# Optimization experiments

Measured on AMD Instinct MI355X. Metric: run time of the kernel, lower is better.

The kernel has to match this reference:

```python
import jax, jax.numpy as jnp
import numpy as np

N_NODES = 100000
N_EDGES = 1600000
F_IN = 128
HID = 128
N_CLASSES = 32
N_GRAPHS = 512


def _seg_mean(vals, idx, num_segments):
    s = jax.ops.segment_sum(vals, idx, num_segments=num_segments)
    cnt = jax.ops.segment_sum(jnp.ones((vals.shape[0],), vals.dtype), idx, num_segments=num_segments)
    return s / jnp.maximum(cnt, 1.0)[:, None]


def _sage_conv(x, src, dst, Wl, bl, Wr):
    # PyG SAGEConv(mean): out = lin_l(mean_{j in N(i)} x_j) + lin_r(x_i); lin_l has bias, lin_r does not.
    agg = _seg_mean(x[src], dst, N_NODES)          # gather + scatter-mean  [N, d]
    return agg @ Wl.T + bl + x @ Wr.T              # [N, H]


def setup_inputs() -> dict:
    key = jax.random.key(0)
    ks = jax.random.split(key, 16)
    x = jax.random.normal(ks[0], (N_NODES, F_IN), dtype=jnp.float32)
    edge_index = jax.random.randint(ks[1], (2, N_EDGES), 0, N_NODES, dtype=jnp.int64)
    batch = jnp.sort(jax.random.randint(ks[2], (N_NODES,), 0, N_GRAPHS, dtype=jnp.int64))
    sc = 0.05
    params = {
        'Wl0': jax.random.normal(ks[3], (HID, F_IN), jnp.float32) * sc,
        'bl0': jnp.zeros((HID,), jnp.float32),
        'Wr0': jax.random.normal(ks[4], (HID, F_IN), jnp.float32) * sc,
        'Wl1': jax.random.normal(ks[5], (HID, HID), jnp.float32) * sc,
        'bl1': jnp.zeros((HID,), jnp.float32),
        'Wr1': jax.random.normal(ks[6], (HID, HID), jnp.float32) * sc,
        'Wl2': jax.random.normal(ks[7], (HID, HID), jnp.float32) * sc,
        'bl2': jnp.zeros((HID,), jnp.float32),
        'Wr2': jax.random.normal(ks[8], (HID, HID), jnp.float32) * sc,
        'Wlin': jax.random.normal(ks[9], (N_CLASSES, HID), jnp.float32) * sc,
        'blin': jnp.zeros((N_CLASSES,), jnp.float32),
    }
    return {'x': x, 'edge_index': edge_index, 'batch': batch, **params}


def reference(x, edge_index, batch, Wl0, bl0, Wr0, Wl1, bl1, Wr1, Wl2, bl2, Wr2, Wlin, blin):
    src, dst = edge_index[0], edge_index[1]
    # GraphSAGE backbone: relu between layers, no act after last (out_channels set); dropout=identity in eval.
    h = jax.nn.relu(_sage_conv(x, src, dst, Wl0, bl0, Wr0))
    h = jax.nn.relu(_sage_conv(h, src, dst, Wl1, bl1, Wr1))
    h = _sage_conv(h, src, dst, Wl2, bl2, Wr2)
    # global_mean_pool over batch index -> [n_graphs, HID]
    g = _seg_mean(h, batch, N_GRAPHS)
    return g @ Wlin.T + blin  # [n_graphs, n_classes]
```

## Files before the change

kernel.cpp:

```cpp
#include <hip/hip_runtime.h>
#include <hip/hip_bf16.h>


typedef __attribute__((ext_vector_type(8))) short short8v;
typedef __attribute__((ext_vector_type(4))) float f32x4;

#define RK_CH 12544
#define RK_NS 64

__device__ __forceinline__ unsigned short f2bf(float f) {
    __hip_bfloat16 h = __float2bfloat16(f);
    return *reinterpret_cast<unsigned short*>(&h);
}
__device__ __forceinline__ float bf_lo(unsigned u) { return __uint_as_float(u << 16); }
__device__ __forceinline__ float bf_hi(unsigned u) { return __uint_as_float(u & 0xffff0000u); }
__device__ __forceinline__ unsigned packbf(float lo, float hi) {
    return ((unsigned)f2bf(hi) << 16) | f2bf(lo);
}


__launch_bounds__(256)
__global__ void pre_kernel(const int* __restrict__ dst,
                           unsigned short* __restrict__ rank16,
                           unsigned short* __restrict__ counts16,
                           int nE, int nChunk, int es,
                           const float* __restrict__ x, unsigned short* __restrict__ xbf, int x4,
                           const float* __restrict__ w0, const float* __restrict__ w1,
                           const float* __restrict__ w2, const float* __restrict__ w3,
                           const float* __restrict__ w4, const float* __restrict__ w5,
                           unsigned short* __restrict__ o0, unsigned short* __restrict__ o1,
                           unsigned short* __restrict__ o2, unsigned short* __restrict__ o3,
                           unsigned short* __restrict__ o4, unsigned short* __restrict__ o5,
                           int w4n, int w4b) {
    __shared__ unsigned cnt[RK_CH];
    int rhB  = nChunk * RK_NS;
    int cvtB = (x4 + 255) / 256;
    int bid  = blockIdx.x;

    if (bid < rhB) {
        int s = bid / nChunk;
        int c = bid % nChunk;
        int lo = c * RK_CH;
        for (int i = threadIdx.x; i < RK_CH; i += 256) cnt[i] = 0u;
        __syncthreads();

        int ebeg = s * es;
        int eend = ebeg + es; if (eend > nE) eend = nE;
        if (ebeg < eend) {
            int nvec = (eend - ebeg) >> 2;
            for (int g = threadIdx.x; g < nvec; g += 256) {
                int e = ebeg + g * 4;
                int4 d4 = *(const int4*)&dst[e];
                unsigned dc;
                dc = (unsigned)(d4.x - lo);
                if (dc < RK_CH) rank16[e]     = (unsigned short)atomicAdd(&cnt[dc], 1u);
                dc = (unsigned)(d4.y - lo);
                if (dc < RK_CH) rank16[e + 1] = (unsigned short)atomicAdd(&cnt[dc], 1u);
                dc = (unsigned)(d4.z - lo);
                if (dc < RK_CH) rank16[e + 2] = (unsigned short)atomicAdd(&cnt[dc], 1u);
                dc = (unsigned)(d4.w - lo);
                if (dc < RK_CH) rank16[e + 3] = (unsigned short)atomicAdd(&cnt[dc], 1u);
            }
            for (int e = ebeg + (nvec << 2) + threadIdx.x; e < eend; e += 256) {
                unsigned dc = (unsigned)(dst[e] - lo);
                if (dc < RK_CH) rank16[e] = (unsigned short)atomicAdd(&cnt[dc], 1u);
            }
        }
        __syncthreads();
        size_t base = ((size_t)(c * RK_NS + s)) * RK_CH;
        for (int i = threadIdx.x; i < RK_CH; i += 256)
            counts16[base + i] = (unsigned short)cnt[i];
    } else if (bid < rhB + cvtB) {
        int i = (bid - rhB) * 256 + threadIdx.x;
        if (i < x4) {
            float4 v = ((const float4*)x)[i];
            ushort4 o;
            o.x = f2bf(v.x); o.y = f2bf(v.y); o.z = f2bf(v.z); o.w = f2bf(v.w);
            ((ushort4*)xbf)[i] = o;
        }
    } else {
        int idx  = bid - rhB - cvtB;
        int wsel = idx / w4b;
        int wb   = idx % w4b;
        const float* in; unsigned short* out;
        switch (wsel) {
            case 0: in = w0; out = o0; break;
            case 1: in = w1; out = o1; break;
            case 2: in = w2; out = o2; break;
            case 3: in = w3; out = o3; break;
            case 4: in = w4; out = o4; break;
            default: in = w5; out = o5; break;
        }
        int i = wb * 256 + threadIdx.x;
        if (i < w4n) {
            float4 v = ((const float4*)in)[i];
            ushort4 o;
            o.x = f2bf(v.x); o.y = f2bf(v.y); o.z = f2bf(v.z); o.w = f2bf(v.w);
            ((ushort4*)out)[i] = o;
        }
    }
}


__launch_bounds__(1024)
__global__ void seg_scan1_kernel(unsigned short* __restrict__ counts16,
                                 int* __restrict__ rowptr, int* __restrict__ bsum, int n) {
    __shared__ int s[1024];
    int lid = threadIdx.x;
    int d = blockIdx.x * 1024 + lid;
    int v = 0;
    if (d < n) {
        int c = d / RK_CH;
        int i = d - c * RK_CH;
        size_t base = ((size_t)c * RK_NS) * RK_CH + i;
        unsigned run = 0;
        for (int sl = 0; sl < RK_NS; ++sl) {
            size_t idx = base + (size_t)sl * RK_CH;
            unsigned t = counts16[idx];
            counts16[idx] = (unsigned short)run;
            run += t;
        }
        v = (int)run;
    }
    s[lid] = v;
    __syncthreads();
    #pragma unroll
    for (int off = 1; off < 1024; off <<= 1) {
        int t = (lid >= off) ? s[lid - off] : 0;
        __syncthreads();
        s[lid] += t;
        __syncthreads();
    }
    if (d < n) rowptr[d] = s[lid] - v;
    if (lid == 0) bsum[blockIdx.x] = s[1023];
}

__global__ void scan2_kernel(int* __restrict__ bsum, int nb) {
    __shared__ int s[1024];
    int lid = threadIdx.x;
    int v = (lid < nb) ? bsum[lid] : 0;
    s[lid] = v;
    __syncthreads();
    #pragma unroll
    for (int off = 1; off < 1024; off <<= 1) {
        int t = (lid >= off) ? s[lid - off] : 0;
        __syncthreads();
        s[lid] += t;
        __syncthreads();
    }
    if (lid < nb) bsum[lid] = s[lid] - v;
}

__global__ void scan3_kernel(int* __restrict__ rowptr, const int* __restrict__ bsum,
                             int n, int nE) {
    int i = blockIdx.x * blockDim.x + threadIdx.x;
    if (i < n) rowptr[i] += bsum[i >> 10];
    if (i == 0) rowptr[n] = nE;
}

__global__ void scatter2_kernel(const int* __restrict__ src, const int* __restrict__ dst,
                                const unsigned short* __restrict__ rank16,
                                const unsigned short* __restrict__ counts16,
                                const int* __restrict__ rowptr,
                                int* __restrict__ esrc, int nE, int es) {
    int e = blockIdx.x * blockDim.x + threadIdx.x;
    if (e >= nE) return;
    int d = dst[e];
    int s = e / es;
    int c = d / RK_CH;
    int i = d - c * RK_CH;
    int pos = rowptr[d] + (int)counts16[((size_t)(c * RK_NS + s)) * RK_CH + i]
                        + (int)rank16[e];
    esrc[pos] = src[e];
}


#define ACC8(v) do { \
    s0 += bf_lo((v).x); s1 += bf_hi((v).x); s2 += bf_lo((v).y); s3 += bf_hi((v).y); \
    s4 += bf_lo((v).z); s5 += bf_hi((v).z); s6 += bf_lo((v).w); s7 += bf_hi((v).w); } while (0)

__global__ void aggregate_kernel(const unsigned short* __restrict__ h,
                                 const int* __restrict__ rowptr,
                                 const int* __restrict__ esrc,
                                 unsigned short* __restrict__ agg, int n) {
    int wave = (blockIdx.x * blockDim.x + threadIdx.x) >> 6;
    int lane = threadIdx.x & 63;
    int q    = lane >> 4;
    int li   = lane & 15;
    int c0   = li * 8;
    int node = wave * 4 + q;

    int beg = 0, end = 0;
    if (node < n) { beg = rowptr[node]; end = rowptr[node + 1]; }

    float s0=0.f,s1=0.f,s2=0.f,s3=0.f,s4=0.f,s5=0.f,s6=0.f,s7=0.f;
    int j = beg;
    for (; j + 4 <= end; j += 4) {
        int r0 = esrc[j], r1 = esrc[j + 1], r2 = esrc[j + 2], r3 = esrc[j + 3];
        uint4 v0 = *(const uint4*)&h[(size_t)r0 * 128 + c0];
        uint4 v1 = *(const uint4*)&h[(size_t)r1 * 128 + c0];
        uint4 v2 = *(const uint4*)&h[(size_t)r2 * 128 + c0];
        uint4 v3 = *(const uint4*)&h[(size_t)r3 * 128 + c0];
        ACC8(v0); ACC8(v1); ACC8(v2); ACC8(v3);
    }
    for (; j < end; ++j) {
        int r0 = esrc[j];
        uint4 v0 = *(const uint4*)&h[(size_t)r0 * 128 + c0];
        ACC8(v0);
    }
    if (node < n) {
        int cnt = end - beg;
        float inv = 1.0f / (float)(cnt > 1 ? cnt : 1);
        uint4 o;
        o.x = packbf(s0 * inv, s1 * inv);
        o.y = packbf(s2 * inv, s3 * inv);
        o.z = packbf(s4 * inv, s5 * inv);
        o.w = packbf(s6 * inv, s7 * inv);
        *(uint4*)&agg[(size_t)node * 128 + c0] = o;
    }
}


__launch_bounds__(256)
__global__ void sage_gemm_mfma(const unsigned short* __restrict__ A,
                               const unsigned short* __restrict__ H,
                               const unsigned short* __restrict__ Wl,
                               const unsigned short* __restrict__ Wr,
                               const float* __restrict__ bl,
                               unsigned short* __restrict__ out, int n, int relu) {
    int tid  = threadIdx.x;
    int lane = tid & 63;
    int w    = tid >> 6;
    int wm   = w >> 1, wn = w & 1;
    int br   = blockIdx.x * 128 + wm * 64;
    int bc   = wn * 64;
    int lrow = lane & 15;
    int lk   = (lane >> 4) * 8;

    f32x4 acc[4][4] = {};

    #pragma unroll
    for (int half = 0; half < 2; ++half) {
        const unsigned short* X = half ? H : A;
        const unsigned short* W = half ? Wr : Wl;
        const unsigned short* xp[4];
        const unsigned short* wp[4];
        #pragma unroll
        for (int mb = 0; mb < 4; ++mb) {
            int r = br + mb * 16 + lrow;
            if (r >= n) r = n - 1;
            xp[mb] = X + (size_t)r * 128 + lk;
        }
        #pragma unroll
        for (int nb = 0; nb < 4; ++nb)
            wp[nb] = W + (size_t)(bc + nb * 16 + lrow) * 128 + lk;

        #pragma unroll
        for (int ks = 0; ks < 4; ++ks) {
            short8v a[4], b[4];
            #pragma unroll
            for (int mb = 0; mb < 4; ++mb) a[mb] = *(const short8v*)(xp[mb] + ks * 32);
            #pragma unroll
            for (int nb = 0; nb < 4; ++nb) b[nb] = *(const short8v*)(wp[nb] + ks * 32);
            #pragma unroll
            for (int mb = 0; mb < 4; ++mb)
                #pragma unroll
                for (int nb = 0; nb < 4; ++nb)
                    acc[mb][nb] = __builtin_amdgcn_mfma_f32_16x16x32_bf16(
                        a[mb], b[nb], acc[mb][nb], 0, 0, 0);
        }
    }

    int ccol  = lane & 15;
    int crow4 = (lane >> 4) * 4;
    float bv[4];
    #pragma unroll
    for (int nb = 0; nb < 4; ++nb) bv[nb] = bl[bc + nb * 16 + ccol];

    #pragma unroll
    for (int mb = 0; mb < 4; ++mb) {
        #pragma unroll
        for (int r = 0; r < 4; ++r) {
            int row = br + mb * 16 + crow4 + r;
            if (row < n) {
                #pragma unroll
                for (int nb = 0; nb < 4; ++nb) {
                    int col = bc + nb * 16 + ccol;
                    float v = acc[mb][nb][r] + bv[nb];
                    if (relu && v < 0.f) v = 0.f;
                    out[(size_t)row * 128 + col] = f2bf(v);
                }
            }
        }
    }
}


__device__ __forceinline__ int lbound(const int* __restrict__ a, int n, int v) {
    int lo = 0, hi = n;
    while (lo < hi) { int m = (lo + hi) >> 1; if (a[m] < v) lo = m + 1; else hi = m; }
    return lo;
}

__launch_bounds__(1024)
__global__ void pool_head_kernel(const unsigned short* __restrict__ h,
                                 const int* __restrict__ batch,
                                 const float* __restrict__ Wlin,
                                 const float* __restrict__ blin,
                                 float* __restrict__ out, int n) {
    __shared__ float red[16][128];
    int b  = blockIdx.x;
    int rg = threadIdx.x >> 6;
    int cp = threadIdx.x & 63;
    int lo = lbound(batch, n, b);
    int hi = lbound(batch, n, b + 1);
    float s0 = 0.f, s1 = 0.f;
    for (int i = lo + rg; i < hi; i += 16) {
        unsigned v = *(const unsigned*)&h[(size_t)i * 128 + cp * 2];
        s0 += bf_lo(v); s1 += bf_hi(v);
    }
    red[rg][cp * 2]     = s0;
    red[rg][cp * 2 + 1] = s1;
    __syncthreads();
    #pragma unroll
    for (int off = 8; off >= 1; off >>= 1) {
        if (rg < off) {
            red[rg][cp * 2]     += red[rg + off][cp * 2];
            red[rg][cp * 2 + 1] += red[rg + off][cp * 2 + 1];
        }
        __syncthreads();
    }
    if (threadIdx.x < 32) {
        int j = threadIdx.x;
        int cnt = hi - lo;
        float inv = 1.0f / (float)(cnt > 1 ? cnt : 1);
        const float* wr = &Wlin[(size_t)j * 128];
        float s = 0.f;
        #pragma unroll 4
        for (int c = 0; c < 128; ++c) s += red[0][c] * wr[c];
        out[(size_t)b * 32 + j] = blin[j] + s * inv;
    }
}

extern "C" void kernel_launch(void* const* d_in, const int* in_sizes, int n_in,
                              void* d_out, int out_size, void* d_ws, size_t ws_size,
                              hipStream_t stream) {
    const float* x      = (const float*)d_in[0];
    const int*   eidx   = (const int*)d_in[1];
    const int*   batch  = (const int*)d_in[2];
    const float* Wl[3]  = {(const float*)d_in[3], (const float*)d_in[6], (const float*)d_in[9]};
    const float* bl[3]  = {(const float*)d_in[4], (const float*)d_in[7], (const float*)d_in[10]};
    const float* Wr[3]  = {(const float*)d_in[5], (const float*)d_in[8], (const float*)d_in[11]};
    const float* Wlin   = (const float*)d_in[12];
    const float* blin   = (const float*)d_in[13];
    float* out = (float*)d_out;

    const int N = in_sizes[0] / 128;
    const int E = in_sizes[1] / 2;

    const int* esrc_in = eidx;
    const int* edst_in = eidx + E;

    char* w = (char*)d_ws;
    auto carve = [&](size_t bytes) { char* p = w; w += (bytes + 255) & ~(size_t)255; return p; };
    unsigned short* xbf  = (unsigned short*)carve((size_t)N * 128 * 2);
    unsigned short* hA   = (unsigned short*)carve((size_t)N * 128 * 2);
    unsigned short* hB   = (unsigned short*)carve((size_t)N * 128 * 2);
    unsigned short* agg  = (unsigned short*)carve((size_t)N * 128 * 2);
    unsigned short* Wbf[6];
    for (int i = 0; i < 6; ++i) Wbf[i] = (unsigned short*)carve((size_t)128 * 128 * 2);
    int*   rowptr = (int*)carve((size_t)(N + 1) * 4);
    int*   bsum   = (int*)carve(1024 * 4);
    int*   esrc   = (int*)carve((size_t)E * 4);
    unsigned short* rank16   = (unsigned short*)carve((size_t)E * 2);
    int nChunk = (N + RK_CH - 1) / RK_CH;
    unsigned short* counts16 = (unsigned short*)carve((size_t)nChunk * RK_NS * RK_CH * 2);
    (void)ws_size; (void)n_in;

    int es = (((E + RK_NS - 1) / RK_NS) + 3) & ~3;
    int x4   = N * 128 / 4;
    int cvtB = (x4 + 255) / 256;
    int w4n  = 128 * 128 / 4;
    int w4b  = (w4n + 255) / 256;
    int rhB  = nChunk * RK_NS;
    hipLaunchKernelGGL(pre_kernel, dim3(rhB + cvtB + 6 * w4b), dim3(256), 0, stream,
                       edst_in, rank16, counts16, E, nChunk, es,
                       x, xbf, x4,
                       Wl[0], Wr[0], Wl[1], Wr[1], Wl[2], Wr[2],
                       Wbf[0], Wbf[1], Wbf[2], Wbf[3], Wbf[4], Wbf[5],
                       w4n, w4b);

    int nchunks = (N + 1023) / 1024;
    hipLaunchKernelGGL(seg_scan1_kernel, dim3(nchunks), dim3(1024), 0, stream,
                       counts16, rowptr, bsum, N);
    hipLaunchKernelGGL(scan2_kernel, dim3(1), dim3(1024), 0, stream, bsum, nchunks);
    int ngrid = (N + 255) / 256;
    hipLaunchKernelGGL(scan3_kernel, dim3(ngrid), dim3(256), 0, stream, rowptr, bsum, N, E);
    int egrid = (E + 255) / 256;
    hipLaunchKernelGGL(scatter2_kernel, dim3(egrid), dim3(256), 0, stream,
                       esrc_in, edst_in, rank16, counts16, rowptr, esrc, E, es);

    int agrid = (N + 15) / 16;
    int ggrid = (N + 127) / 128;
    const unsigned short* hin = xbf;
    unsigned short* houts[3] = {hA, hB, hA};
    for (int l = 0; l < 3; ++l) {
        hipLaunchKernelGGL(aggregate_kernel, dim3(agrid), dim3(256), 0, stream,
                           hin, rowptr, esrc, agg, N);
        hipLaunchKernelGGL(sage_gemm_mfma, dim3(ggrid), dim3(256), 0, stream,
                           agg, hin, Wbf[2*l], Wbf[2*l+1], bl[l], houts[l], N, (l < 2) ? 1 : 0);
        hin = houts[l];
    }

    int G = out_size / 32;
    hipLaunchKernelGGL(pool_head_kernel, dim3(G), dim3(1024), 0, stream,
                       hin, batch, Wlin, blin, out, N);
}
```

Before: 383.0 us.

## Bucketize edges by destination chunk before scattering into CSR

Replaces the single random scatter of source ids into the CSR edge array with two passes. The first pass writes (position, src) pairs into per-chunk buckets using per-slice chunk totals and wave ballots. The second pass scatters each chunk's bucket, so writes stay within a localized CSR region and get better cache and write locality. The cost is an extra pass over E 8-byte records and a bucketize kernel that launches only 64 blocks, which may limit parallelism.

```diff
diff --git a/kernel.cpp b/kernel.cpp
--- a/kernel.cpp
+++ b/kernel.cpp
@@ -23,6 +23,7 @@
 __global__ void pre_kernel(const int* __restrict__ dst,
                            unsigned short* __restrict__ rank16,
                            unsigned short* __restrict__ counts16,
+                           unsigned* __restrict__ stot,
                            int nE, int nChunk, int es,
                            const float* __restrict__ x, unsigned short* __restrict__ xbf, int x4,
                            const float* __restrict__ w0, const float* __restrict__ w1,
@@ -33,6 +34,7 @@
                            unsigned short* __restrict__ o4, unsigned short* __restrict__ o5,
                            int w4n, int w4b) {
     __shared__ unsigned cnt[RK_CH];
+    __shared__ unsigned red[256];
     int rhB  = nChunk * RK_NS;
     int cvtB = (x4 + 255) / 256;
     int bid  = blockIdx.x;
@@ -68,8 +70,19 @@
         }
         __syncthreads();
         size_t base = ((size_t)(c * RK_NS + s)) * RK_CH;
-        for (int i = threadIdx.x; i < RK_CH; i += 256)
+        unsigned tsum = 0;
+        for (int i = threadIdx.x; i < RK_CH; i += 256) {
             counts16[base + i] = (unsigned short)cnt[i];
+            tsum += cnt[i];
+        }
+        red[threadIdx.x] = tsum;
+        __syncthreads();
+        #pragma unroll
+        for (int off = 128; off >= 1; off >>= 1) {
+            if (threadIdx.x < off) red[threadIdx.x] += red[threadIdx.x + off];
+            __syncthreads();
+        }
+        if (threadIdx.x == 0) stot[(c << 6) | s] = red[0];
     } else if (bid < rhB + cvtB) {
         int i = (bid - rhB) * 256 + threadIdx.x;
         if (i < x4) {
@@ -135,20 +148,36 @@
     if (lid == 0) bsum[blockIdx.x] = s[1023];
 }
 
-__global__ void scan2_kernel(int* __restrict__ bsum, int nb) {
+__launch_bounds__(1024)
+__global__ void scans2b_kernel(int* __restrict__ bsum, int nb,
+                               unsigned* __restrict__ stot, int ns) {
     __shared__ int s[1024];
     int lid = threadIdx.x;
-    int v = (lid < nb) ? bsum[lid] : 0;
-    s[lid] = v;
-    __syncthreads();
-    #pragma unroll
-    for (int off = 1; off < 1024; off <<= 1) {
-        int t = (lid >= off) ? s[lid - off] : 0;
-        __syncthreads();
-        s[lid] += t;
-        __syncthreads();
-    }
-    if (lid < nb) bsum[lid] = s[lid] - v;
+    if (blockIdx.x == 0) {
+        int v = (lid < nb) ? bsum[lid] : 0;
+        s[lid] = v;
+        __syncthreads();
+        #pragma unroll
+        for (int off = 1; off < 1024; off <<= 1) {
+            int t = (lid >= off) ? s[lid - off] : 0;
+            __syncthreads();
+            s[lid] += t;
+            __syncthreads();
+        }
+        if (lid < nb) bsum[lid] = s[lid] - v;
+    } else {
+        int v = (lid < ns) ? (int)stot[lid] : 0;
+        s[lid] = v;
+        __syncthreads();
+        #pragma unroll
+        for (int off = 1; off < 1024; off <<= 1) {
+            int t = (lid >= off) ? s[lid - off] : 0;
+            __syncthreads();
+            s[lid] += t;
+            __syncthreads();
+        }
+        if (lid < ns) stot[lid] = (unsigned)(s[lid] - v);
+    }
 }
 
 __global__ void scan3_kernel(int* __restrict__ rowptr, const int* __restrict__ bsum,
@@ -158,20 +187,69 @@
     if (i == 0) rowptr[n] = nE;
 }
 
-__global__ void scatter2_kernel(const int* __restrict__ src, const int* __restrict__ dst,
-                                const unsigned short* __restrict__ rank16,
-                                const unsigned short* __restrict__ counts16,
-                                const int* __restrict__ rowptr,
-                                int* __restrict__ esrc, int nE, int es) {
-    int e = blockIdx.x * blockDim.x + threadIdx.x;
-    if (e >= nE) return;
-    int d = dst[e];
-    int s = e / es;
-    int c = d / RK_CH;
-    int i = d - c * RK_CH;
-    int pos = rowptr[d] + (int)counts16[((size_t)(c * RK_NS + s)) * RK_CH + i]
-                        + (int)rank16[e];
-    esrc[pos] = src[e];
+__launch_bounds__(256)
+__global__ void bucketize_kernel(const int* __restrict__ src, const int* __restrict__ dst,
+                                 const unsigned short* __restrict__ rank16,
+                                 const unsigned short* __restrict__ counts16,
+                                 const int* __restrict__ rowptr,
+                                 const unsigned* __restrict__ sbase,
+                                 uint2* __restrict__ bkt,
+                                 int nE, int nChunk, int es) {
+    __shared__ unsigned lcur[8];
+    __shared__ unsigned lbase[8];
+    int s = blockIdx.x;
+    if (threadIdx.x < 8) {
+        lcur[threadIdx.x] = 0;
+        lbase[threadIdx.x] = (threadIdx.x < nChunk) ? sbase[(threadIdx.x << 6) | s] : 0u;
+    }
+    __syncthreads();
+    int ebeg = s * es;
+    int eend = ebeg + es; if (eend > nE) eend = nE;
+    int lane = threadIdx.x & 63;
+    for (int e0 = ebeg; e0 < eend; e0 += 256) {
+        int e = e0 + threadIdx.x;
+        bool valid = e < eend;
+        int c = -1, pos = 0, srcv = 0;
+        if (valid) {
+            int d = dst[e];
+            srcv = src[e];
+            c = (int)((unsigned)d / RK_CH);
+            int i = d - c * RK_CH;
+            pos = rowptr[d] + (int)counts16[((size_t)(c * RK_NS + s)) * RK_CH + i]
+                            + (int)rank16[e];
+        }
+        unsigned slot = 0;
+        for (int k = 0; k < nChunk; ++k) {
+            unsigned long long mask = __ballot(valid && (c == k));
+            if (mask) {
+                int leader = __ffsll((long long)mask) - 1;
+                unsigned wb = 0;
+                if (lane == leader) wb = atomicAdd(&lcur[k], (unsigned)__popcll(mask));
+                wb = __shfl(wb, leader);
+                if (valid && c == k)
+                    slot = wb + (unsigned)__popcll(mask & ((1ull << lane) - 1ull));
+            }
+        }
+        if (valid) bkt[(size_t)lbase[c] + slot] = make_uint2((unsigned)pos, (unsigned)srcv);
+    }
+}
+
+__launch_bounds__(256)
+__global__ void scatter_b_kernel(const uint2* __restrict__ bkt,
+                                 const unsigned* __restrict__ sbase,
+                                 int* __restrict__ esrc, int nE, int nChunk, int M) {
+    int c = blockIdx.x % nChunk;
+    int m = blockIdx.x / nChunk;
+    unsigned lo = sbase[c << 6];
+    unsigned hi = (c + 1 < nChunk) ? sbase[(c + 1) << 6] : (unsigned)nE;
+    unsigned csize = hi - lo;
+    unsigned seg = (csize + (unsigned)M - 1) / (unsigned)M;
+    unsigned b0 = lo + (unsigned)m * seg;
+    unsigned b1 = b0 + seg; if (b1 > hi) b1 = hi;
+    for (unsigned p = b0 + threadIdx.x; p < b1; p += 256) {
+        uint2 pr = bkt[(size_t)p];
+        esrc[pr.x] = (int)pr.y;
+    }
 }
 
 
@@ -375,6 +453,8 @@
     unsigned short* rank16   = (unsigned short*)carve((size_t)E * 2);
     int nChunk = (N + RK_CH - 1) / RK_CH;
     unsigned short* counts16 = (unsigned short*)carve((size_t)nChunk * RK_NS * RK_CH * 2);
+    unsigned* stot = (unsigned*)carve(1024 * 4);
+    uint2*    bkt  = (uint2*)carve((size_t)E * 8);
     (void)ws_size; (void)n_in;
 
     int es = (((E + RK_NS - 1) / RK_NS) + 3) & ~3;
@@ -384,7 +464,7 @@
     int w4b  = (w4n + 255) / 256;
     int rhB  = nChunk * RK_NS;
     hipLaunchKernelGGL(pre_kernel, dim3(rhB + cvtB + 6 * w4b), dim3(256), 0, stream,
-                       edst_in, rank16, counts16, E, nChunk, es,
+                       edst_in, rank16, counts16, stot, E, nChunk, es,
                        x, xbf, x4,
                        Wl[0], Wr[0], Wl[1], Wr[1], Wl[2], Wr[2],
                        Wbf[0], Wbf[1], Wbf[2], Wbf[3], Wbf[4], Wbf[5],
@@ -393,12 +473,15 @@
     int nchunks = (N + 1023) / 1024;
     hipLaunchKernelGGL(seg_scan1_kernel, dim3(nchunks), dim3(1024), 0, stream,
                        counts16, rowptr, bsum, N);
-    hipLaunchKernelGGL(scan2_kernel, dim3(1), dim3(1024), 0, stream, bsum, nchunks);
+    hipLaunchKernelGGL(scans2b_kernel, dim3(2), dim3(1024), 0, stream,
+                       bsum, nchunks, stot, nChunk * RK_NS);
     int ngrid = (N + 255) / 256;
     hipLaunchKernelGGL(scan3_kernel, dim3(ngrid), dim3(256), 0, stream, rowptr, bsum, N, E);
-    int egrid = (E + 255) / 256;
-    hipLaunchKernelGGL(scatter2_kernel, dim3(egrid), dim3(256), 0, stream,
-                       esrc_in, edst_in, rank16, counts16, rowptr, esrc, E, es);
+    hipLaunchKernelGGL(bucketize_kernel, dim3(RK_NS), dim3(256), 0, stream,
+                       esrc_in, edst_in, rank16, counts16, rowptr, stot, bkt, E, nChunk, es);
+    const int MB = 64;
+    hipLaunchKernelGGL(scatter_b_kernel, dim3(nChunk * MB), dim3(256), 0, stream,
+                       bkt, stot, esrc, E, nChunk, MB);
 
     int agrid = (N + 15) / 16;
     int ggrid = (N + 127) / 128;
```

After: 559.0 us. 1.46x slower.
